# Kernel optimization log

Measured on AMD Instinct MI355X. Metric: run time of the kernel, lower is better.

Reference implementation:

```python
import jax, jax.numpy as jnp
import numpy as np

D = 512
H = 8
HD = D // H
EPS = 1e-5
NEG_INF = -1e30


def _ln(x, g, b):
    mu = jnp.mean(x, axis=-1, keepdims=True)
    var = jnp.mean(jnp.square(x - mu), axis=-1, keepdims=True)
    return (x - mu) * jax.lax.rsqrt(var + EPS) * g + b


def setup_inputs() -> dict:
    key = jax.random.key(0)
    ks = jax.random.split(key, 8)
    V, M, S = 128, 128, 514  # seq includes 2 head tokens (cls+dist)
    inp = {
        "video_embeds": jax.random.normal(ks[0], (V, D), jnp.float32),
        "music_features": jax.random.normal(ks[1], (M, S, D), jnp.float32),
        "music_masks": jnp.ones((M, S - 2), jnp.int32),
    }
    wk = jax.random.split(ks[2], 5)
    for name, k in zip(["Wq", "Wk", "Wv", "Wo", "Wl"], wk):
        inp[name] = jax.random.normal(k, (D, D), jnp.float32) * 0.02
    for name in ["bq", "bk", "bv", "bo", "bl"]:
        inp[name] = jnp.zeros((D,), jnp.float32)
    for name in ["g1", "g2", "g3"]:
        inp[name] = jnp.ones((D,), jnp.float32)
    for name in ["b1", "b2", "b3"]:
        inp[name] = jnp.zeros((D,), jnp.float32)
    return inp


def reference(video_embeds, music_features, music_masks,
              Wq, bq, Wk, bk, Wv, bv, Wo, bo, Wl, bl,
              g1, b1, g2, b2, g3, b3):
    # drop cls + dist tokens
    mf = music_features[:, 2:, :]  # (M, f, D)
    ve = _ln(video_embeds, g1, b1)  # (V, D)
    mf = _ln(mf, g1, b1)
    V = ve.shape[0]
    M, f, _ = mf.shape

    q = (ve @ Wq.T + bq).reshape(V, H, HD).transpose(1, 0, 2)        # (H, V, hd)
    k = (mf @ Wk.T + bk).reshape(M, f, H, HD).transpose(0, 2, 1, 3)  # (M, H, f, hd)
    v = (mf @ Wv.T + bv).reshape(M, f, H, HD).transpose(0, 2, 1, 3)  # (M, H, f, hd)

    logits = jnp.einsum('hvd,mhfd->vmhf', q, k) / np.sqrt(HD).astype(np.float32)
    mask = music_masks[None, :, None, :]  # (1, M, 1, f)
    logits = jnp.where(mask == 0, NEG_INF, logits)
    w = jax.nn.softmax(logits, axis=-1)
    attn = jnp.einsum('vmhf,mhfd->vmhd', w, v).reshape(V, M, D)
    attn = attn @ Wo.T + bo

    attn = _ln(attn, g2, b2)
    out = attn + (attn @ Wl.T + bl)  # dropout = identity in eval
    return _ln(out, g3, b3)
```

## Files before the change

### kernel.cpp

```cpp
#include <hip/hip_runtime.h>
#include <hip/hip_bf16.h>

typedef unsigned int uint;
typedef unsigned short ushort;
typedef __bf16 bf16;
typedef bf16 bf16x8 __attribute__((ext_vector_type(8)));
typedef float f32x4 __attribute__((ext_vector_type(4)));
typedef ushort ushort4v __attribute__((ext_vector_type(4)));

__device__ __forceinline__ float bf2f(ushort u) {
  union { uint u; float f; } v; v.u = ((uint)u) << 16; return v.f;
}
__device__ __forceinline__ ushort f2bf(float f) {
  union { float f; uint u; } v; v.f = f;
  uint u = v.u;
  uint r = (u + 0x7fffu + ((u >> 16) & 1u)) >> 16;
  return (ushort)r;
}

__device__ __forceinline__ void gl2lds16(const void* g, void* l) {
  __builtin_amdgcn_global_load_lds(
      (const __attribute__((address_space(1))) void*)g,
      (__attribute__((address_space(3))) void*)l, 16, 0, 0);
}

__device__ __forceinline__ void ln_rows(
    int mode, int nrows, int blk, int nblk, int tid,
    const void* __restrict__ srcA, const void* __restrict__ srcB,
    const float* __restrict__ g, const float* __restrict__ b,
    void* __restrict__ dst)
{
  const int l = tid & 63;
  const int nw = nblk * 4;
  for (int row = blk * 4 + (tid >> 6); row < nrows; row += nw) {
    float x[8];
    if (mode <= 1) {
      const float* s;
      if (mode == 0) {
        s = (const float*)srcA + (size_t)row * 512;
      } else {
        int mm = row >> 9, fi = row & 511;
        s = (const float*)srcA + ((size_t)mm * 514 + 2 + fi) * 512;
      }
      float4 a0 = *(const float4*)(s + l * 4);
      float4 a1 = *(const float4*)(s + 256 + l * 4);
      x[0] = a0.x; x[1] = a0.y; x[2] = a0.z; x[3] = a0.w;
      x[4] = a1.x; x[5] = a1.y; x[6] = a1.z; x[7] = a1.w;
    } else if (mode == 2) {
      const ushort* s = (const ushort*)srcA + (size_t)row * 512;
      uint4 u = *(const uint4*)(s + l * 8);
      x[0] = bf2f((ushort)u.x); x[1] = bf2f((ushort)(u.x >> 16));
      x[2] = bf2f((ushort)u.y); x[3] = bf2f((ushort)(u.y >> 16));
      x[4] = bf2f((ushort)u.z); x[5] = bf2f((ushort)(u.z >> 16));
      x[6] = bf2f((ushort)u.w); x[7] = bf2f((ushort)(u.w >> 16));
    } else {
      const ushort* sa = (const ushort*)srcA + (size_t)row * 512;
      const ushort* sb = (const ushort*)srcB + (size_t)row * 512;
      uint4 ua = *(const uint4*)(sa + l * 8);
      uint4 ub = *(const uint4*)(sb + l * 8);
      x[0] = bf2f((ushort)ua.x) + bf2f((ushort)ub.x);
      x[1] = bf2f((ushort)(ua.x >> 16)) + bf2f((ushort)(ub.x >> 16));
      x[2] = bf2f((ushort)ua.y) + bf2f((ushort)ub.y);
      x[3] = bf2f((ushort)(ua.y >> 16)) + bf2f((ushort)(ub.y >> 16));
      x[4] = bf2f((ushort)ua.z) + bf2f((ushort)ub.z);
      x[5] = bf2f((ushort)(ua.z >> 16)) + bf2f((ushort)(ub.z >> 16));
      x[6] = bf2f((ushort)ua.w) + bf2f((ushort)ub.w);
      x[7] = bf2f((ushort)(ua.w >> 16)) + bf2f((ushort)(ub.w >> 16));
    }
    float sum = 0.f, sq = 0.f;
    #pragma unroll
    for (int j = 0; j < 8; ++j) { sum += x[j]; sq += x[j] * x[j]; }
    #pragma unroll
    for (int o = 1; o < 64; o <<= 1) {
      sum += __shfl_xor(sum, o);
      sq  += __shfl_xor(sq, o);
    }
    const float inv = 1.f / 512.f;
    float mu = sum * inv;
    float var = sq * inv - mu * mu;
    float rstd = rsqrtf(var + 1e-5f);

    float gv[8], bv[8];
    if (mode <= 1) {
      float4 g0 = *(const float4*)(g + l * 4);
      float4 g1 = *(const float4*)(g + 256 + l * 4);
      float4 b0 = *(const float4*)(b + l * 4);
      float4 b1 = *(const float4*)(b + 256 + l * 4);
      gv[0] = g0.x; gv[1] = g0.y; gv[2] = g0.z; gv[3] = g0.w;
      gv[4] = g1.x; gv[5] = g1.y; gv[6] = g1.z; gv[7] = g1.w;
      bv[0] = b0.x; bv[1] = b0.y; bv[2] = b0.z; bv[3] = b0.w;
      bv[4] = b1.x; bv[5] = b1.y; bv[6] = b1.z; bv[7] = b1.w;
    } else {
      float4 g0 = *(const float4*)(g + l * 8);
      float4 g1 = *(const float4*)(g + l * 8 + 4);
      float4 b0 = *(const float4*)(b + l * 8);
      float4 b1 = *(const float4*)(b + l * 8 + 4);
      gv[0] = g0.x; gv[1] = g0.y; gv[2] = g0.z; gv[3] = g0.w;
      gv[4] = g1.x; gv[5] = g1.y; gv[6] = g1.z; gv[7] = g1.w;
      bv[0] = b0.x; bv[1] = b0.y; bv[2] = b0.z; bv[3] = b0.w;
      bv[4] = b1.x; bv[5] = b1.y; bv[6] = b1.z; bv[7] = b1.w;
    }
    float y[8];
    #pragma unroll
    for (int j = 0; j < 8; ++j) y[j] = (x[j] - mu) * rstd * gv[j] + bv[j];

    if (mode <= 1) {
      ushort* d = (ushort*)dst + (size_t)row * 512;
      ushort4v p0, p1;
      #pragma unroll
      for (int j = 0; j < 4; ++j) { p0[j] = f2bf(y[j]); p1[j] = f2bf(y[4 + j]); }
      *(ushort4v*)(d + l * 4) = p0;
      *(ushort4v*)(d + 256 + l * 4) = p1;
    } else if (mode == 2) {
      ushort* d = (ushort*)dst + (size_t)row * 512;
      uint4 o;
      o.x = (uint)f2bf(y[0]) | ((uint)f2bf(y[1]) << 16);
      o.y = (uint)f2bf(y[2]) | ((uint)f2bf(y[3]) << 16);
      o.z = (uint)f2bf(y[4]) | ((uint)f2bf(y[5]) << 16);
      o.w = (uint)f2bf(y[6]) | ((uint)f2bf(y[7]) << 16);
      *(uint4*)(d + l * 8) = o;
    } else {
      float* d = (float*)dst + (size_t)row * 512;
      float4 o0, o1;
      o0.x = y[0]; o0.y = y[1]; o0.z = y[2]; o0.w = y[3];
      o1.x = y[4]; o1.y = y[5]; o1.z = y[6]; o1.w = y[7];
      *(float4*)(d + l * 8) = o0;
      *(float4*)(d + l * 8 + 4) = o1;
    }
  }
}

__global__ __launch_bounds__(256) void ln512v(
    int mode, int nrows,
    const void* __restrict__ srcA, const void* __restrict__ srcB,
    const float* __restrict__ g, const float* __restrict__ b,
    void* __restrict__ dst)
{
  ln_rows(mode, nrows, blockIdx.x, gridDim.x, threadIdx.x, srcA, srcB, g, b, dst);
}

struct PreArgs {
  const float* s0; const float* s1; const float* s2; const float* s3; const float* s4;
  ushort* d0; ushort* d1; ushort* d2; ushort* d3; ushort* d4;
  const float* video; const float* music;
  const float* g1; const float* b1;
  ushort* veln; ushort* mfln;
};
__global__ __launch_bounds__(256) void preamble(PreArgs a) {
  int bb = blockIdx.x;
  if (bb < 640) {
    int t = bb * 256 + threadIdx.x;
    int which = t >> 15;
    int e = (t & 32767) * 8;
    const float* s = which == 0 ? a.s0 : which == 1 ? a.s1 : which == 2 ? a.s2 : which == 3 ? a.s3 : a.s4;
    ushort*      d = which == 0 ? a.d0 : which == 1 ? a.d1 : which == 2 ? a.d2 : which == 3 ? a.d3 : a.d4;
    float4 v0 = *(const float4*)(s + e);
    float4 v1 = *(const float4*)(s + e + 4);
    uint4 o;
    o.x = (uint)f2bf(v0.x) | ((uint)f2bf(v0.y) << 16);
    o.y = (uint)f2bf(v0.z) | ((uint)f2bf(v0.w) << 16);
    o.z = (uint)f2bf(v1.x) | ((uint)f2bf(v1.y) << 16);
    o.w = (uint)f2bf(v1.z) | ((uint)f2bf(v1.w) << 16);
    *(uint4*)(d + e) = o;
  } else if (bb < 672) {
    ln_rows(0, 128, bb - 640, 32, threadIdx.x, a.video, nullptr, a.g1, a.b1, a.veln);
  } else {
    ln_rows(1, 65536, bb - 672, 2048, threadIdx.x, a.music, nullptr, a.g1, a.b1, a.mfln);
  }
}

__global__ __launch_bounds__(256) void gemm_t3(
    const ushort* __restrict__ A, const ushort* __restrict__ W,
    const float* __restrict__ bias, ushort* __restrict__ C,
    float scale, int vt_mode)
{
  __shared__ __align__(16) ushort As[2][128 * 64];
  __shared__ __align__(16) ushort Bs[2][128 * 64];
  const int tid = threadIdx.x;
  const int w = tid >> 6, l = tid & 63;
  const int lg = l >> 4, lr = l & 15;
  const int wr = w >> 1, wc = w & 1;

  int nwg = gridDim.x * gridDim.y;
  int bid = blockIdx.y * gridDim.x + blockIdx.x;
  if ((nwg & 7) == 0) bid = (bid & 7) * (nwg >> 3) + (bid >> 3);
  const int bx = bid % gridDim.x, by = bid / gridDim.x;
  const int row0 = by * 128, col0 = bx * 128;

  f32x4 acc[4][4];
  #pragma unroll
  for (int i = 0; i < 4; i++)
    #pragma unroll
    for (int j = 0; j < 4; j++) { f32x4 z = {0.f,0.f,0.f,0.f}; acc[i][j] = z; }

  size_t asrc[4], wsrc[4]; int ldst[4];
  #pragma unroll
  for (int c2 = 0; c2 < 4; ++c2) {
    int c = c2 * 256 + tid;
    int r = c >> 3, j = c & 7;
    int koff = (j ^ (r & 7)) * 8;
    asrc[c2] = (size_t)(row0 + r) * 512 + koff;
    wsrc[c2] = (size_t)(col0 + r) * 512 + koff;
    ldst[c2] = (c2 * 256 + w * 64) * 8;
  }

  auto stage = [&](int pb, int kk) {
    #pragma unroll
    for (int c2 = 0; c2 < 4; ++c2) {
      gl2lds16(A + asrc[c2] + kk * 64, &As[pb][ldst[c2]]);
      gl2lds16(W + wsrc[c2] + kk * 64, &Bs[pb][ldst[c2]]);
    }
  };
  auto compute = [&](int pb) {
    #pragma unroll
    for (int ks = 0; ks < 2; ++ks) {
      bf16x8 af[4], bfr[4];
      #pragma unroll
      for (int mi = 0; mi < 4; ++mi) {
        int r = wr * 64 + mi * 16 + lr;
        af[mi] = *(const bf16x8*)(&As[pb][r * 64 + ((ks * 32 + lg * 8) ^ ((r & 7) * 8))]);
      }
      #pragma unroll
      for (int ni = 0; ni < 4; ++ni) {
        int r = wc * 64 + ni * 16 + lr;
        bfr[ni] = *(const bf16x8*)(&Bs[pb][r * 64 + ((ks * 32 + lg * 8) ^ ((r & 7) * 8))]);
      }
      #pragma unroll
      for (int mi = 0; mi < 4; ++mi)
        #pragma unroll
        for (int ni = 0; ni < 4; ++ni)
          acc[mi][ni] = __builtin_amdgcn_mfma_f32_16x16x32_bf16(af[mi], bfr[ni], acc[mi][ni], 0, 0, 0);
    }
  };

  stage(0, 0);
  __syncthreads();
  int cur = 0;
  #pragma unroll
  for (int kk = 0; kk < 7; ++kk) {
    stage(cur ^ 1, kk + 1);
    compute(cur);
    __syncthreads();
    cur ^= 1;
  }
  compute(cur);

  #pragma unroll
  for (int ni = 0; ni < 4; ++ni) {
    int cg = col0 + wc * 64 + ni * 16 + lr;
    float bc = bias[cg];
    #pragma unroll
    for (int mi = 0; mi < 4; ++mi) {
      int rg0 = row0 + wr * 64 + mi * 16 + lg * 4;
      if (!vt_mode) {
        #pragma unroll
        for (int e = 0; e < 4; ++e) {
          float v = (acc[mi][ni][e] + bc) * scale;
          C[(size_t)(rg0 + e) * 512 + cg] = f2bf(v);
        }
      } else {
        int m = rg0 >> 9, fi = rg0 & 511;
        ushort4v pk;
        #pragma unroll
        for (int e = 0; e < 4; ++e) pk[e] = f2bf((acc[mi][ni][e] + bc) * scale);
        *(ushort4v*)(C + (size_t)(m * 512 + cg) * 512 + fi) = pk;
      }
    }
  }
}

__global__ __launch_bounds__(256) void attn_kernel(
    const ushort* __restrict__ q, const ushort* __restrict__ k,
    const ushort* __restrict__ vt, const int* __restrict__ masks,
    ushort* __restrict__ attn)
{
  __shared__ __align__(16) ushort Qs[128 * 64];
  __shared__ __align__(16) ushort Ks[64 * 64];
  __shared__ __align__(16) ushort Vs[64 * 64];
  __shared__ __align__(16) ushort Ps[4][32 * 64];
  __shared__ float maskf[64];
  __shared__ float stats[4][32];

  const int tid = threadIdx.x;
  const int w = tid >> 6, l = tid & 63;
  const int lg = l >> 4, lr = l & 15;
  const int m = blockIdx.x >> 3, h = blockIdx.x & 7;

  const size_t kbase = (size_t)(m * 512) * 512 + h * 64;
  const size_t vbase = (size_t)(m * 512 + h * 64) * 512;

  #pragma unroll
  for (int c2 = 0; c2 < 4; ++c2) {
    int c = c2 * 256 + tid;
    int r = c >> 3, j = c & 7;
    gl2lds16(q + (size_t)r * 512 + h * 64 + ((j * 8) ^ ((r & 7) * 8)),
             Qs + (c2 * 256 + w * 64) * 8);
  }

  f32x4 acc[2][4];
  #pragma unroll
  for (int i = 0; i < 2; i++)
    #pragma unroll
    for (int j = 0; j < 4; j++) { f32x4 z = {0.f,0.f,0.f,0.f}; acc[i][j] = z; }
  float m_run[2] = {-INFINITY, -INFINITY};
  float l_run[2] = {0.f, 0.f};
  bf16x8 qf[2][2];

  for (int it = 0; it < 8; ++it) {
    const int f0 = it * 64;
    #pragma unroll
    for (int c2 = 0; c2 < 2; ++c2) {
      int c = c2 * 256 + tid;
      int r = c >> 3, j = c & 7;
      int off = (j * 8) ^ ((r & 7) * 8);
      gl2lds16(k + kbase + (size_t)(f0 + r) * 512 + off, Ks + (c2 * 256 + w * 64) * 8);
      gl2lds16(vt + vbase + (size_t)r * 512 + f0 + off, Vs + (c2 * 256 + w * 64) * 8);
    }
    if (tid < 64) maskf[tid] = masks[m * 512 + f0 + tid] ? 0.f : -1e30f;
    __syncthreads();

    if (it == 0) {
      #pragma unroll
      for (int nv = 0; nv < 2; ++nv)
        #pragma unroll
        for (int k2 = 0; k2 < 2; ++k2) {
          int v = w * 32 + nv * 16 + lr;
          qf[nv][k2] = *(const bf16x8*)(Qs + v * 64 + ((k2 * 32 + lg * 8) ^ ((v & 7) * 8)));
        }
    }

    f32x4 s[4][2];
    #pragma unroll
    for (int mi = 0; mi < 4; mi++)
      #pragma unroll
      for (int nv = 0; nv < 2; nv++) { f32x4 z = {0.f,0.f,0.f,0.f}; s[mi][nv] = z; }
    #pragma unroll
    for (int k2 = 0; k2 < 2; ++k2) {
      bf16x8 kf[4];
      #pragma unroll
      for (int mi = 0; mi < 4; ++mi) {
        int f = mi * 16 + lr;
        kf[mi] = *(const bf16x8*)(Ks + f * 64 + ((k2 * 32 + lg * 8) ^ ((f & 7) * 8)));
      }
      __builtin_amdgcn_s_setprio(1);
      #pragma unroll
      for (int mi = 0; mi < 4; ++mi)
        #pragma unroll
        for (int nv = 0; nv < 2; ++nv)
          s[mi][nv] = __builtin_amdgcn_mfma_f32_16x16x32_bf16(kf[mi], qf[nv][k2], s[mi][nv], 0, 0, 0);
      __builtin_amdgcn_s_setprio(0);
    }

    float mk[4][4];
    #pragma unroll
    for (int mi = 0; mi < 4; mi++)
      #pragma unroll
      for (int e = 0; e < 4; e++) mk[mi][e] = maskf[mi * 16 + lg * 4 + e];

    #pragma unroll
    for (int nv = 0; nv < 2; ++nv) {
      float cmax = -INFINITY;
      #pragma unroll
      for (int mi = 0; mi < 4; mi++)
        #pragma unroll
        for (int e = 0; e < 4; e++) {
          s[mi][nv][e] += mk[mi][e];
          cmax = fmaxf(cmax, s[mi][nv][e]);
        }
      cmax = fmaxf(cmax, __shfl_xor(cmax, 16));
      cmax = fmaxf(cmax, __shfl_xor(cmax, 32));
      float mnew = fmaxf(m_run[nv], cmax);
      float sc = __expf(m_run[nv] - mnew);
      float csum = 0.f;
      int vloc = nv * 16 + lr;
      #pragma unroll
      for (int mi = 0; mi < 4; mi++) {
        ushort4v pk;
        #pragma unroll
        for (int e = 0; e < 4; e++) {
          float p = __expf(s[mi][nv][e] - mnew);
          csum += p;
          pk[e] = f2bf(p);
        }
        int f = mi * 16 + lg * 4;
        *(ushort4v*)(&Ps[w][vloc * 64 + (f ^ ((vloc & 7) * 8))]) = pk;
      }
      csum += __shfl_xor(csum, 16);
      csum += __shfl_xor(csum, 32);
      l_run[nv] = l_run[nv] * sc + csum;
      m_run[nv] = mnew;
      if (lg == 0) stats[w][vloc] = sc;
    }

    #pragma unroll
    for (int mi2 = 0; mi2 < 2; ++mi2)
      #pragma unroll
      for (int e = 0; e < 4; ++e) {
        float sc = stats[w][mi2 * 16 + lg * 4 + e];
        #pragma unroll
        for (int nd = 0; nd < 4; ++nd) acc[mi2][nd][e] *= sc;
      }

    #pragma unroll
    for (int k2 = 0; k2 < 2; ++k2) {
      bf16x8 pf[2], vf[4];
      #pragma unroll
      for (int mi2 = 0; mi2 < 2; ++mi2) {
        int vloc = mi2 * 16 + lr;
        pf[mi2] = *(const bf16x8*)(&Ps[w][vloc * 64 + ((k2 * 32 + lg * 8) ^ ((vloc & 7) * 8))]);
      }
      #pragma unroll
      for (int nd = 0; nd < 4; ++nd) {
        int d = nd * 16 + lr;
        vf[nd] = *(const bf16x8*)(Vs + d * 64 + ((k2 * 32 + lg * 8) ^ ((d & 7) * 8)));
      }
      __builtin_amdgcn_s_setprio(1);
      #pragma unroll
      for (int mi2 = 0; mi2 < 2; ++mi2)
        #pragma unroll
        for (int nd = 0; nd < 4; ++nd)
          acc[mi2][nd] = __builtin_amdgcn_mfma_f32_16x16x32_bf16(pf[mi2], vf[nd], acc[mi2][nd], 0, 0, 0);
      __builtin_amdgcn_s_setprio(0);
    }
    __syncthreads();
  }

  #pragma unroll
  for (int nv = 0; nv < 2; ++nv)
    if (lg == 0) stats[w][nv * 16 + lr] = 1.f / l_run[nv];
  #pragma unroll
  for (int mi2 = 0; mi2 < 2; ++mi2)
    #pragma unroll
    for (int e = 0; e < 4; ++e) {
      float invl = stats[w][mi2 * 16 + lg * 4 + e];
      int vg = w * 32 + mi2 * 16 + lg * 4 + e;
      #pragma unroll
      for (int nd = 0; nd < 4; ++nd) {
        int d = nd * 16 + lr;
        attn[(size_t)(vg * 128 + m) * 512 + h * 64 + d] = f2bf(acc[mi2][nd][e] * invl);
      }
    }
}

extern "C" void kernel_launch(void* const* d_in, const int* in_sizes, int n_in,
                              void* d_out, int out_size, void* d_ws, size_t ws_size,
                              hipStream_t stream) {
  const float* video = (const float*)d_in[0];
  const float* music = (const float*)d_in[1];
  const int*   masks = (const int*)d_in[2];
  const float* Wq = (const float*)d_in[3];
  const float* Wk = (const float*)d_in[4];
  const float* Wv = (const float*)d_in[5];
  const float* Wo = (const float*)d_in[6];
  const float* Wl = (const float*)d_in[7];
  const float* bq = (const float*)d_in[8];
  const float* bk = (const float*)d_in[9];
  const float* bv = (const float*)d_in[10];
  const float* bo = (const float*)d_in[11];
  const float* bl = (const float*)d_in[12];
  const float* g1 = (const float*)d_in[13];
  const float* g2 = (const float*)d_in[14];
  const float* g3 = (const float*)d_in[15];
  const float* b1 = (const float*)d_in[16];
  const float* b2 = (const float*)d_in[17];
  const float* b3 = (const float*)d_in[18];

  char* ws = (char*)d_ws;
  ushort* mfln = (ushort*)(ws);
  ushort* kbuf = (ushort*)(ws + 67108864);
  ushort* vtb  = (ushort*)(ws + 134217728);
  ushort* attn = (ushort*)(ws + 201326592);
  ushort* c1   = (ushort*)(ws + 218103808);
  ushort* xbuf = (ushort*)(ws + 234881024);
  ushort* veln = (ushort*)(ws + 251658240);
  ushort* qbuf = (ushort*)(ws + 251789312);
  ushort* wqb  = (ushort*)(ws + 251920384);
  ushort* wkb  = wqb + 262144;
  ushort* wvb  = wkb + 262144;
  ushort* wob  = wvb + 262144;
  ushort* wlb  = wob + 262144;

  PreArgs pa = {Wq, Wk, Wv, Wo, Wl, wqb, wkb, wvb, wob, wlb,
                video, music, g1, b1, veln, mfln};
  preamble<<<2720, 256, 0, stream>>>(pa);

  gemm_t3<<<dim3(4, 1), 256, 0, stream>>>(veln, wqb, bq, qbuf, 0.125f, 0);
  gemm_t3<<<dim3(4, 512), 256, 0, stream>>>(mfln, wkb, bk, kbuf, 1.f, 0);
  gemm_t3<<<dim3(4, 512), 256, 0, stream>>>(mfln, wvb, bv, vtb, 1.f, 1);

  attn_kernel<<<1024, 256, 0, stream>>>(qbuf, kbuf, vtb, masks, attn);

  gemm_t3<<<dim3(4, 128), 256, 0, stream>>>(attn, wob, bo, c1, 1.f, 0);
  ln512v<<<2048, 256, 0, stream>>>(2, 16384, c1, nullptr, g2, b2, xbuf);
  gemm_t3<<<dim3(4, 128), 256, 0, stream>>>(xbuf, wlb, bl, c1, 1.f, 0);
  ln512v<<<2048, 256, 0, stream>>>(3, 16384, xbuf, c1, g3, b3, d_out);
}
```

Baseline: 282.3 us.

## Stage GEMM epilogue through LDS, merge Q into K GEMM, pair-row layernorms

The GEMM epilogue now writes the tile into LDS with an XOR swizzle and then issues coalesced 16-byte global stores, in both normal and transposed-V modes, instead of scattered 2-byte or 8-byte stores. The small Q projection is folded into the K projection launch as an extra grid row, which removes one launch. Layernorm kernels now process two rows per wave with no grid-stride loop, and the preamble grid is sized to match. The staging adds an extra barrier and LDS traffic per tile, and the layernorm change trades loop overhead for more blocks.

New measurement: 328.8 us. 1.16x slower.

```diff
diff --git a/kernel.cpp b/kernel.cpp
--- a/kernel.cpp
+++ b/kernel.cpp
@@ -24,119 +24,203 @@
       (__attribute__((address_space(3))) void*)l, 16, 0, 0);
 }
 
-__device__ __forceinline__ void ln_rows(
-    int mode, int nrows, int blk, int nblk, int tid,
+__device__ __forceinline__ void ln_rows0(
+    int nrows, int blk, int nblk, int tid,
+    const float* __restrict__ srcA,
+    const float* __restrict__ g, const float* __restrict__ b,
+    ushort* __restrict__ dst)
+{
+  const int l = tid & 63;
+  const int nw = nblk * 4;
+  for (int row = blk * 4 + (tid >> 6); row < nrows; row += nw) {
+    const float* s = srcA + (size_t)row * 512;
+    float x[8];
+    float4 a0 = *(const float4*)(s + l * 4);
+    float4 a1 = *(const float4*)(s + 256 + l * 4);
+    x[0] = a0.x; x[1] = a0.y; x[2] = a0.z; x[3] = a0.w;
+    x[4] = a1.x; x[5] = a1.y; x[6] = a1.z; x[7] = a1.w;
+    float sum = 0.f, sq = 0.f;
+    #pragma unroll
+    for (int j = 0; j < 8; ++j) { sum += x[j]; sq += x[j] * x[j]; }
+    #pragma unroll
+    for (int o = 1; o < 64; o <<= 1) {
+      sum += __shfl_xor(sum, o);
+      sq  += __shfl_xor(sq, o);
+    }
+    float mu = sum * (1.f / 512.f);
+    float var = sq * (1.f / 512.f) - mu * mu;
+    float rstd = rsqrtf(var + 1e-5f);
+    float4 g0 = *(const float4*)(g + l * 4);
+    float4 g1 = *(const float4*)(g + 256 + l * 4);
+    float4 b0 = *(const float4*)(b + l * 4);
+    float4 b1 = *(const float4*)(b + 256 + l * 4);
+    float gv[8] = {g0.x,g0.y,g0.z,g0.w,g1.x,g1.y,g1.z,g1.w};
+    float bv[8] = {b0.x,b0.y,b0.z,b0.w,b1.x,b1.y,b1.z,b1.w};
+    ushort* d = dst + (size_t)row * 512;
+    ushort4v p0, p1;
+    #pragma unroll
+    for (int j = 0; j < 4; ++j) {
+      p0[j] = f2bf((x[j] - mu) * rstd * gv[j] + bv[j]);
+      p1[j] = f2bf((x[4+j] - mu) * rstd * gv[4+j] + bv[4+j]);
+    }
+    *(ushort4v*)(d + l * 4) = p0;
+    *(ushort4v*)(d + 256 + l * 4) = p1;
+  }
+}
+
+__device__ __forceinline__ void ln_pair(
+    int mode, int wid, int tid,
     const void* __restrict__ srcA, const void* __restrict__ srcB,
     const float* __restrict__ g, const float* __restrict__ b,
     void* __restrict__ dst)
 {
   const int l = tid & 63;
-  const int nw = nblk * 4;
-  for (int row = blk * 4 + (tid >> 6); row < nrows; row += nw) {
-    float x[8];
-    if (mode <= 1) {
-      const float* s;
-      if (mode == 0) {
-        s = (const float*)srcA + (size_t)row * 512;
-      } else {
-        int mm = row >> 9, fi = row & 511;
-        s = (const float*)srcA + ((size_t)mm * 514 + 2 + fi) * 512;
-      }
-      float4 a0 = *(const float4*)(s + l * 4);
-      float4 a1 = *(const float4*)(s + 256 + l * 4);
-      x[0] = a0.x; x[1] = a0.y; x[2] = a0.z; x[3] = a0.w;
-      x[4] = a1.x; x[5] = a1.y; x[6] = a1.z; x[7] = a1.w;
-    } else if (mode == 2) {
-      const ushort* s = (const ushort*)srcA + (size_t)row * 512;
-      uint4 u = *(const uint4*)(s + l * 8);
-      x[0] = bf2f((ushort)u.x); x[1] = bf2f((ushort)(u.x >> 16));
-      x[2] = bf2f((ushort)u.y); x[3] = bf2f((ushort)(u.y >> 16));
-      x[4] = bf2f((ushort)u.z); x[5] = bf2f((ushort)(u.z >> 16));
-      x[6] = bf2f((ushort)u.w); x[7] = bf2f((ushort)(u.w >> 16));
-    } else {
-      const ushort* sa = (const ushort*)srcA + (size_t)row * 512;
-      const ushort* sb = (const ushort*)srcB + (size_t)row * 512;
-      uint4 ua = *(const uint4*)(sa + l * 8);
-      uint4 ub = *(const uint4*)(sb + l * 8);
-      x[0] = bf2f((ushort)ua.x) + bf2f((ushort)ub.x);
-      x[1] = bf2f((ushort)(ua.x >> 16)) + bf2f((ushort)(ub.x >> 16));
-      x[2] = bf2f((ushort)ua.y) + bf2f((ushort)ub.y);
-      x[3] = bf2f((ushort)(ua.y >> 16)) + bf2f((ushort)(ub.y >> 16));
-      x[4] = bf2f((ushort)ua.z) + bf2f((ushort)ub.z);
-      x[5] = bf2f((ushort)(ua.z >> 16)) + bf2f((ushort)(ub.z >> 16));
-      x[6] = bf2f((ushort)ua.w) + bf2f((ushort)ub.w);
-      x[7] = bf2f((ushort)(ua.w >> 16)) + bf2f((ushort)(ub.w >> 16));
-    }
-    float sum = 0.f, sq = 0.f;
-    #pragma unroll
-    for (int j = 0; j < 8; ++j) { sum += x[j]; sq += x[j] * x[j]; }
-    #pragma unroll
-    for (int o = 1; o < 64; o <<= 1) {
-      sum += __shfl_xor(sum, o);
-      sq  += __shfl_xor(sq, o);
-    }
-    const float inv = 1.f / 512.f;
-    float mu = sum * inv;
-    float var = sq * inv - mu * mu;
-    float rstd = rsqrtf(var + 1e-5f);
-
-    float gv[8], bv[8];
-    if (mode <= 1) {
-      float4 g0 = *(const float4*)(g + l * 4);
-      float4 g1 = *(const float4*)(g + 256 + l * 4);
-      float4 b0 = *(const float4*)(b + l * 4);
-      float4 b1 = *(const float4*)(b + 256 + l * 4);
-      gv[0] = g0.x; gv[1] = g0.y; gv[2] = g0.z; gv[3] = g0.w;
-      gv[4] = g1.x; gv[5] = g1.y; gv[6] = g1.z; gv[7] = g1.w;
-      bv[0] = b0.x; bv[1] = b0.y; bv[2] = b0.z; bv[3] = b0.w;
-      bv[4] = b1.x; bv[5] = b1.y; bv[6] = b1.z; bv[7] = b1.w;
-    } else {
-      float4 g0 = *(const float4*)(g + l * 8);
-      float4 g1 = *(const float4*)(g + l * 8 + 4);
-      float4 b0 = *(const float4*)(b + l * 8);
-      float4 b1 = *(const float4*)(b + l * 8 + 4);
-      gv[0] = g0.x; gv[1] = g0.y; gv[2] = g0.z; gv[3] = g0.w;
-      gv[4] = g1.x; gv[5] = g1.y; gv[6] = g1.z; gv[7] = g1.w;
-      bv[0] = b0.x; bv[1] = b0.y; bv[2] = b0.z; bv[3] = b0.w;
-      bv[4] = b1.x; bv[5] = b1.y; bv[6] = b1.z; bv[7] = b1.w;
-    }
-    float y[8];
-    #pragma unroll
-    for (int j = 0; j < 8; ++j) y[j] = (x[j] - mu) * rstd * gv[j] + bv[j];
-
-    if (mode <= 1) {
-      ushort* d = (ushort*)dst + (size_t)row * 512;
-      ushort4v p0, p1;
-      #pragma unroll
-      for (int j = 0; j < 4; ++j) { p0[j] = f2bf(y[j]); p1[j] = f2bf(y[4 + j]); }
-      *(ushort4v*)(d + l * 4) = p0;
-      *(ushort4v*)(d + 256 + l * 4) = p1;
-    } else if (mode == 2) {
-      ushort* d = (ushort*)dst + (size_t)row * 512;
-      uint4 o;
-      o.x = (uint)f2bf(y[0]) | ((uint)f2bf(y[1]) << 16);
-      o.y = (uint)f2bf(y[2]) | ((uint)f2bf(y[3]) << 16);
-      o.z = (uint)f2bf(y[4]) | ((uint)f2bf(y[5]) << 16);
-      o.w = (uint)f2bf(y[6]) | ((uint)f2bf(y[7]) << 16);
-      *(uint4*)(d + l * 8) = o;
-    } else {
-      float* d = (float*)dst + (size_t)row * 512;
-      float4 o0, o1;
-      o0.x = y[0]; o0.y = y[1]; o0.z = y[2]; o0.w = y[3];
-      o1.x = y[4]; o1.y = y[5]; o1.z = y[6]; o1.w = y[7];
-      *(float4*)(d + l * 8) = o0;
-      *(float4*)(d + l * 8 + 4) = o1;
-    }
-  }
-}
-
-__global__ __launch_bounds__(256) void ln512v(
-    int mode, int nrows,
-    const void* __restrict__ srcA, const void* __restrict__ srcB,
+  const int r0 = wid * 2, r1 = r0 + 1;
+  float x0[8], x1[8];
+  if (mode == 1) {
+    int mm0 = r0 >> 9, fi0 = r0 & 511;
+    int mm1 = r1 >> 9, fi1 = r1 & 511;
+    const float* s0 = (const float*)srcA + ((size_t)mm0 * 514 + 2 + fi0) * 512;
+    const float* s1 = (const float*)srcA + ((size_t)mm1 * 514 + 2 + fi1) * 512;
+    float4 a0 = *(const float4*)(s0 + l * 4);
+    float4 a1 = *(const float4*)(s0 + 256 + l * 4);
+    float4 c0 = *(const float4*)(s1 + l * 4);
+    float4 c1 = *(const float4*)(s1 + 256 + l * 4);
+    x0[0]=a0.x; x0[1]=a0.y; x0[2]=a0.z; x0[3]=a0.w;
+    x0[4]=a1.x; x0[5]=a1.y; x0[6]=a1.z; x0[7]=a1.w;
+    x1[0]=c0.x; x1[1]=c0.y; x1[2]=c0.z; x1[3]=c0.w;
+    x1[4]=c1.x; x1[5]=c1.y; x1[6]=c1.z; x1[7]=c1.w;
+  } else if (mode == 2) {
+    const ushort* s0 = (const ushort*)srcA + (size_t)r0 * 512;
+    const ushort* s1 = (const ushort*)srcA + (size_t)r1 * 512;
+    uint4 u0 = *(const uint4*)(s0 + l * 8);
+    uint4 u1 = *(const uint4*)(s1 + l * 8);
+    x0[0]=bf2f((ushort)u0.x); x0[1]=bf2f((ushort)(u0.x>>16));
+    x0[2]=bf2f((ushort)u0.y); x0[3]=bf2f((ushort)(u0.y>>16));
+    x0[4]=bf2f((ushort)u0.z); x0[5]=bf2f((ushort)(u0.z>>16));
+    x0[6]=bf2f((ushort)u0.w); x0[7]=bf2f((ushort)(u0.w>>16));
+    x1[0]=bf2f((ushort)u1.x); x1[1]=bf2f((ushort)(u1.x>>16));
+    x1[2]=bf2f((ushort)u1.y); x1[3]=bf2f((ushort)(u1.y>>16));
+    x1[4]=bf2f((ushort)u1.z); x1[5]=bf2f((ushort)(u1.z>>16));
+    x1[6]=bf2f((ushort)u1.w); x1[7]=bf2f((ushort)(u1.w>>16));
+  } else {
+    const ushort* sa0 = (const ushort*)srcA + (size_t)r0 * 512;
+    const ushort* sb0 = (const ushort*)srcB + (size_t)r0 * 512;
+    const ushort* sa1 = (const ushort*)srcA + (size_t)r1 * 512;
+    const ushort* sb1 = (const ushort*)srcB + (size_t)r1 * 512;
+    uint4 ua0 = *(const uint4*)(sa0 + l * 8);
+    uint4 ub0 = *(const uint4*)(sb0 + l * 8);
+    uint4 ua1 = *(const uint4*)(sa1 + l * 8);
+    uint4 ub1 = *(const uint4*)(sb1 + l * 8);
+    x0[0]=bf2f((ushort)ua0.x)+bf2f((ushort)ub0.x);
+    x0[1]=bf2f((ushort)(ua0.x>>16))+bf2f((ushort)(ub0.x>>16));
+    x0[2]=bf2f((ushort)ua0.y)+bf2f((ushort)ub0.y);
+    x0[3]=bf2f((ushort)(ua0.y>>16))+bf2f((ushort)(ub0.y>>16));
+    x0[4]=bf2f((ushort)ua0.z)+bf2f((ushort)ub0.z);
+    x0[5]=bf2f((ushort)(ua0.z>>16))+bf2f((ushort)(ub0.z>>16));
+    x0[6]=bf2f((ushort)ua0.w)+bf2f((ushort)ub0.w);
+    x0[7]=bf2f((ushort)(ua0.w>>16))+bf2f((ushort)(ub0.w>>16));
+    x1[0]=bf2f((ushort)ua1.x)+bf2f((ushort)ub1.x);
+    x1[1]=bf2f((ushort)(ua1.x>>16))+bf2f((ushort)(ub1.x>>16));
+    x1[2]=bf2f((ushort)ua1.y)+bf2f((ushort)ub1.y);
+    x1[3]=bf2f((ushort)(ua1.y>>16))+bf2f((ushort)(ub1.y>>16));
+    x1[4]=bf2f((ushort)ua1.z)+bf2f((ushort)ub1.z);
+    x1[5]=bf2f((ushort)(ua1.z>>16))+bf2f((ushort)(ub1.z>>16));
+    x1[6]=bf2f((ushort)ua1.w)+bf2f((ushort)ub1.w);
+    x1[7]=bf2f((ushort)(ua1.w>>16))+bf2f((ushort)(ub1.w>>16));
+  }
+  float s0 = 0.f, q0 = 0.f, s1 = 0.f, q1 = 0.f;
+  #pragma unroll
+  for (int j = 0; j < 8; ++j) {
+    s0 += x0[j]; q0 += x0[j] * x0[j];
+    s1 += x1[j]; q1 += x1[j] * x1[j];
+  }
+  #pragma unroll
+  for (int o = 1; o < 64; o <<= 1) {
+    s0 += __shfl_xor(s0, o); q0 += __shfl_xor(q0, o);
+    s1 += __shfl_xor(s1, o); q1 += __shfl_xor(q1, o);
+  }
+  float mu0 = s0 * (1.f/512.f), mu1 = s1 * (1.f/512.f);
+  float rstd0 = rsqrtf(q0 * (1.f/512.f) - mu0 * mu0 + 1e-5f);
+  float rstd1 = rsqrtf(q1 * (1.f/512.f) - mu1 * mu1 + 1e-5f);
+
+  float gv[8], bv[8];
+  if (mode == 1) {
+    float4 g0 = *(const float4*)(g + l * 4);
+    float4 g1v = *(const float4*)(g + 256 + l * 4);
+    float4 b0 = *(const float4*)(b + l * 4);
+    float4 b1v = *(const float4*)(b + 256 + l * 4);
+    gv[0]=g0.x; gv[1]=g0.y; gv[2]=g0.z; gv[3]=g0.w;
+    gv[4]=g1v.x; gv[5]=g1v.y; gv[6]=g1v.z; gv[7]=g1v.w;
+    bv[0]=b0.x; bv[1]=b0.y; bv[2]=b0.z; bv[3]=b0.w;
+    bv[4]=b1v.x; bv[5]=b1v.y; bv[6]=b1v.z; bv[7]=b1v.w;
+  } else {
+    float4 g0 = *(const float4*)(g + l * 8);
+    float4 g1v = *(const float4*)(g + l * 8 + 4);
+    float4 b0 = *(const float4*)(b + l * 8);
+    float4 b1v = *(const float4*)(b + l * 8 + 4);
+    gv[0]=g0.x; gv[1]=g0.y; gv[2]=g0.z; gv[3]=g0.w;
+    gv[4]=g1v.x; gv[5]=g1v.y; gv[6]=g1v.z; gv[7]=g1v.w;
+    bv[0]=b0.x; bv[1]=b0.y; bv[2]=b0.z; bv[3]=b0.w;
+    bv[4]=b1v.x; bv[5]=b1v.y; bv[6]=b1v.z; bv[7]=b1v.w;
+  }
+  if (mode == 1) {
+    ushort* d0 = (ushort*)dst + (size_t)r0 * 512;
+    ushort* d1 = (ushort*)dst + (size_t)r1 * 512;
+    ushort4v p00, p01, p10, p11;
+    #pragma unroll
+    for (int j = 0; j < 4; ++j) {
+      p00[j] = f2bf((x0[j]-mu0)*rstd0*gv[j]+bv[j]);
+      p01[j] = f2bf((x0[4+j]-mu0)*rstd0*gv[4+j]+bv[4+j]);
+      p10[j] = f2bf((x1[j]-mu1)*rstd1*gv[j]+bv[j]);
+      p11[j] = f2bf((x1[4+j]-mu1)*rstd1*gv[4+j]+bv[4+j]);
+    }
+    *(ushort4v*)(d0 + l * 4) = p00;
+    *(ushort4v*)(d0 + 256 + l * 4) = p01;
+    *(ushort4v*)(d1 + l * 4) = p10;
+    *(ushort4v*)(d1 + 256 + l * 4) = p11;
+  } else if (mode == 2) {
+    ushort* d0 = (ushort*)dst + (size_t)r0 * 512;
+    ushort* d1 = (ushort*)dst + (size_t)r1 * 512;
+    uint4 o0, o1;
+    float y;
+    uint t;
+    y = (x0[0]-mu0)*rstd0*gv[0]+bv[0]; t = f2bf(y);
+    o0.x = t | ((uint)f2bf((x0[1]-mu0)*rstd0*gv[1]+bv[1]) << 16);
+    o0.y = (uint)f2bf((x0[2]-mu0)*rstd0*gv[2]+bv[2]) | ((uint)f2bf((x0[3]-mu0)*rstd0*gv[3]+bv[3]) << 16);
+    o0.z = (uint)f2bf((x0[4]-mu0)*rstd0*gv[4]+bv[4]) | ((uint)f2bf((x0[5]-mu0)*rstd0*gv[5]+bv[5]) << 16);
+    o0.w = (uint)f2bf((x0[6]-mu0)*rstd0*gv[6]+bv[6]) | ((uint)f2bf((x0[7]-mu0)*rstd0*gv[7]+bv[7]) << 16);
+    o1.x = (uint)f2bf((x1[0]-mu1)*rstd1*gv[0]+bv[0]) | ((uint)f2bf((x1[1]-mu1)*rstd1*gv[1]+bv[1]) << 16);
+    o1.y = (uint)f2bf((x1[2]-mu1)*rstd1*gv[2]+bv[2]) | ((uint)f2bf((x1[3]-mu1)*rstd1*gv[3]+bv[3]) << 16);
+    o1.z = (uint)f2bf((x1[4]-mu1)*rstd1*gv[4]+bv[4]) | ((uint)f2bf((x1[5]-mu1)*rstd1*gv[5]+bv[5]) << 16);
+    o1.w = (uint)f2bf((x1[6]-mu1)*rstd1*gv[6]+bv[6]) | ((uint)f2bf((x1[7]-mu1)*rstd1*gv[7]+bv[7]) << 16);
+    *(uint4*)(d0 + l * 8) = o0;
+    *(uint4*)(d1 + l * 8) = o1;
+  } else {
+    float* d0 = (float*)dst + (size_t)r0 * 512;
+    float* d1 = (float*)dst + (size_t)r1 * 512;
+    float4 a0, a1, c0, c1;
+    a0.x=(x0[0]-mu0)*rstd0*gv[0]+bv[0]; a0.y=(x0[1]-mu0)*rstd0*gv[1]+bv[1];
+    a0.z=(x0[2]-mu0)*rstd0*gv[2]+bv[2]; a0.w=(x0[3]-mu0)*rstd0*gv[3]+bv[3];
+    a1.x=(x0[4]-mu0)*rstd0*gv[4]+bv[4]; a1.y=(x0[5]-mu0)*rstd0*gv[5]+bv[5];
+    a1.z=(x0[6]-mu0)*rstd0*gv[6]+bv[6]; a1.w=(x0[7]-mu0)*rstd0*gv[7]+bv[7];
+    c0.x=(x1[0]-mu1)*rstd1*gv[0]+bv[0]; c0.y=(x1[1]-mu1)*rstd1*gv[1]+bv[1];
+    c0.z=(x1[2]-mu1)*rstd1*gv[2]+bv[2]; c0.w=(x1[3]-mu1)*rstd1*gv[3]+bv[3];
+    c1.x=(x1[4]-mu1)*rstd1*gv[4]+bv[4]; c1.y=(x1[5]-mu1)*rstd1*gv[5]+bv[5];
+    c1.z=(x1[6]-mu1)*rstd1*gv[6]+bv[6]; c1.w=(x1[7]-mu1)*rstd1*gv[7]+bv[7];
+    *(float4*)(d0 + l * 8) = a0;
+    *(float4*)(d0 + l * 8 + 4) = a1;
+    *(float4*)(d1 + l * 8) = c0;
+    *(float4*)(d1 + l * 8 + 4) = c1;
+  }
+}
+
+__global__ __launch_bounds__(256) void ln512p(
+    int mode, const void* __restrict__ srcA, const void* __restrict__ srcB,
     const float* __restrict__ g, const float* __restrict__ b,
     void* __restrict__ dst)
 {
-  ln_rows(mode, nrows, blockIdx.x, gridDim.x, threadIdx.x, srcA, srcB, g, b, dst);
+  ln_pair(mode, blockIdx.x * 4 + (threadIdx.x >> 6), threadIdx.x, srcA, srcB, g, b, dst);
 }
 
 struct PreArgs {
@@ -163,16 +247,19 @@
     o.w = (uint)f2bf(v1.z) | ((uint)f2bf(v1.w) << 16);
     *(uint4*)(d + e) = o;
   } else if (bb < 672) {
-    ln_rows(0, 128, bb - 640, 32, threadIdx.x, a.video, nullptr, a.g1, a.b1, a.veln);
+    ln_rows0(128, bb - 640, 32, threadIdx.x, a.video, a.g1, a.b1, a.veln);
   } else {
-    ln_rows(1, 65536, bb - 672, 2048, threadIdx.x, a.music, nullptr, a.g1, a.b1, a.mfln);
+    ln_pair(1, (bb - 672) * 4 + (threadIdx.x >> 6), threadIdx.x,
+            a.music, nullptr, a.g1, a.b1, a.mfln);
   }
 }
 
 __global__ __launch_bounds__(256) void gemm_t3(
     const ushort* __restrict__ A, const ushort* __restrict__ W,
     const float* __restrict__ bias, ushort* __restrict__ C,
-    float scale, int vt_mode)
+    float scale, int vt_mode,
+    const ushort* __restrict__ Aq, const ushort* __restrict__ Wqp,
+    const float* __restrict__ bqp, ushort* __restrict__ Qout, int qy)
 {
   __shared__ __align__(16) ushort As[2][128 * 64];
   __shared__ __align__(16) ushort Bs[2][128 * 64];
@@ -181,11 +268,18 @@
   const int lg = l >> 4, lr = l & 15;
   const int wr = w >> 1, wc = w & 1;
 
-  int nwg = gridDim.x * gridDim.y;
-  int bid = blockIdx.y * gridDim.x + blockIdx.x;
-  if ((nwg & 7) == 0) bid = (bid & 7) * (nwg >> 3) + (bid >> 3);
-  const int bx = bid % gridDim.x, by = bid / gridDim.x;
-  const int row0 = by * 128, col0 = bx * 128;
+  int row0, col0;
+  const bool isq = ((int)blockIdx.y == qy);
+  if (isq) {
+    A = Aq; W = Wqp; bias = bqp; C = Qout; scale = 0.125f; vt_mode = 0;
+    row0 = 0; col0 = blockIdx.x * 128;
+  } else {
+    int nwg = gridDim.x * (qy >= 0 ? qy : gridDim.y);
+    int bid = blockIdx.y * gridDim.x + blockIdx.x;
+    if ((nwg & 7) == 0) bid = (bid & 7) * (nwg >> 3) + (bid >> 3);
+    row0 = (bid / gridDim.x) * 128;
+    col0 = (bid % gridDim.x) * 128;
+  }
 
   f32x4 acc[4][4];
   #pragma unroll
@@ -244,27 +338,38 @@
     cur ^= 1;
   }
   compute(cur);
-
+  __syncthreads();
+
+  ushort* img = (ushort*)As;
   #pragma unroll
   for (int ni = 0; ni < 4; ++ni) {
-    int cg = col0 + wc * 64 + ni * 16 + lr;
-    float bc = bias[cg];
+    float bc = bias[col0 + wc * 64 + ni * 16 + lr];
     #pragma unroll
     for (int mi = 0; mi < 4; ++mi) {
-      int rg0 = row0 + wr * 64 + mi * 16 + lg * 4;
-      if (!vt_mode) {
-        #pragma unroll
-        for (int e = 0; e < 4; ++e) {
-          float v = (acc[mi][ni][e] + bc) * scale;
-          C[(size_t)(rg0 + e) * 512 + cg] = f2bf(v);
-        }
-      } else {
-        int m = rg0 >> 9, fi = rg0 & 511;
-        ushort4v pk;
-        #pragma unroll
-        for (int e = 0; e < 4; ++e) pk[e] = f2bf((acc[mi][ni][e] + bc) * scale);
-        *(ushort4v*)(C + (size_t)(m * 512 + cg) * 512 + fi) = pk;
-      }
+      #pragma unroll
+      for (int e = 0; e < 4; ++e) {
+        float v = (acc[mi][ni][e] + bc) * scale;
+        int x, y;
+        if (!vt_mode) { x = wr * 64 + mi * 16 + lg * 4 + e; y = wc * 64 + ni * 16 + lr; }
+        else          { x = wc * 64 + ni * 16 + lr;         y = wr * 64 + mi * 16 + lg * 4 + e; }
+        int byte = x * 256 + ((y * 2) ^ (((x >> 2) & 3) * 32));
+        img[byte >> 1] = f2bf(v);
+      }
+    }
+  }
+  __syncthreads();
+  {
+    const int m = row0 >> 9, fi0 = row0 & 511;
+    #pragma unroll
+    for (int pass = 0; pass < 8; ++pass) {
+      int r = pass * 16 + (tid >> 4);
+      int cb = tid & 15;
+      int byte = r * 256 + ((cb * 16) ^ (((r >> 2) & 3) * 32));
+      uint4 d = *(const uint4*)(img + (byte >> 1));
+      if (!vt_mode)
+        *(uint4*)(C + (size_t)(row0 + r) * 512 + col0 + cb * 8) = d;
+      else
+        *(uint4*)(C + (size_t)(m * 512 + col0 + r) * 512 + fi0 + cb * 8) = d;
     }
   }
 }
@@ -482,16 +587,19 @@
 
   PreArgs pa = {Wq, Wk, Wv, Wo, Wl, wqb, wkb, wvb, wob, wlb,
                 video, music, g1, b1, veln, mfln};
-  preamble<<<2720, 256, 0, stream>>>(pa);
-
-  gemm_t3<<<dim3(4, 1), 256, 0, stream>>>(veln, wqb, bq, qbuf, 0.125f, 0);
-  gemm_t3<<<dim3(4, 512), 256, 0, stream>>>(mfln, wkb, bk, kbuf, 1.f, 0);
-  gemm_t3<<<dim3(4, 512), 256, 0, stream>>>(mfln, wvb, bv, vtb, 1.f, 1);
+  preamble<<<8864, 256, 0, stream>>>(pa);
+
+  gemm_t3<<<dim3(4, 513), 256, 0, stream>>>(
+      mfln, wkb, bk, kbuf, 1.f, 0, veln, wqb, bq, qbuf, 512);
+  gemm_t3<<<dim3(4, 512), 256, 0, stream>>>(
+      mfln, wvb, bv, vtb, 1.f, 1, nullptr, nullptr, nullptr, nullptr, -1);
 
   attn_kernel<<<1024, 256, 0, stream>>>(qbuf, kbuf, vtb, masks, attn);
 
-  gemm_t3<<<dim3(4, 128), 256, 0, stream>>>(attn, wob, bo, c1, 1.f, 0);
-  ln512v<<<2048, 256, 0, stream>>>(2, 16384, c1, nullptr, g2, b2, xbuf);
-  gemm_t3<<<dim3(4, 128), 256, 0, stream>>>(xbuf, wlb, bl, c1, 1.f, 0);
-  ln512v<<<2048, 256, 0, stream>>>(3, 16384, xbuf, c1, g3, b3, d_out);
-}
+  gemm_t3<<<dim3(4, 128), 256, 0, stream>>>(
+      attn, wob, bo, c1, 1.f, 0, nullptr, nullptr, nullptr, nullptr, -1);
+  ln512p<<<2048, 256, 0, stream>>>(2, c1, nullptr, g2, b2, xbuf);
+  gemm_t3<<<dim3(4, 128), 256, 0, stream>>>(
+      xbuf, wlb, bl, c1, 1.f, 0, nullptr, nullptr, nullptr, nullptr, -1);
+  ln512p<<<2048, 256, 0, stream>>>(3, xbuf, c1, g3, b3, d_out);
+}
```
